# Kernel tuning notes

Hardware: AMD Instinct MI355X
Metric: run time of the kernel (lower is better)

Reference implementation:

```python
import jax, jax.numpy as jnp
import numpy as np

B = 1024      # batch of seed nodes
S = 16        # sample_size
H = 256       # hidden
IN = 150      # in_dim + NUM_CLASS (128 + 22)
OUT = 22
HEADS = 8
NN = 100000   # number of graph nodes
LN_EPS = 1e-5


def setup_inputs() -> dict:
    key = jax.random.key(0)
    ks = jax.random.split(key, 16)
    sc = 0.05
    return {
        "node_feats": jax.random.normal(ks[0], (NN, IN), jnp.float32),
        "batch": jax.random.randint(ks[1], (B,), 0, NN),
        "nbr2": jax.random.randint(ks[2], (B, S), 0, NN),
        "nbr1": jax.random.randint(ks[3], (B * (S + 1), S), 0, NN),
        "W_in": jax.random.normal(ks[4], (IN, H), jnp.float32) * sc,
        "b_in": jnp.zeros((H,), jnp.float32),
        "Wqkv": jax.random.normal(ks[5], (2, 3, H, H), jnp.float32) * sc,
        "bqkv": jnp.zeros((2, 3, H), jnp.float32),
        "Wo": jax.random.normal(ks[6], (2, H, H), jnp.float32) * sc,
        "bo": jnp.zeros((2, H), jnp.float32),
        "Wf": jax.random.normal(ks[7], (2, H, H), jnp.float32) * sc,
        "bf": jnp.zeros((2, H), jnp.float32),
        "ln_g": jnp.ones((4, H), jnp.float32),
        "ln_b": jnp.zeros((4, H), jnp.float32),
        "W_out": jax.random.normal(ks[8], (H, OUT), jnp.float32) * sc,
        "b_out": jnp.zeros((OUT,), jnp.float32),
    }


def _layer_norm(x, g, b):
    m = jnp.mean(x, axis=-1, keepdims=True)
    v = jnp.mean((x - m) ** 2, axis=-1, keepdims=True)
    return (x - m) * jax.lax.rsqrt(v + LN_EPS) * g + b


def _mha(q, kv, Wq, Wk, Wv, bq, bk, bv, Wout, bout):
    # q: [N, 1, H], kv: [N, S, H]; single-query multi-head attention
    N, Sk, _ = kv.shape
    dh = H // HEADS
    qp = (q @ Wq + bq).reshape(N, 1, HEADS, dh)
    kp = (kv @ Wk + bk).reshape(N, Sk, HEADS, dh)
    vp = (kv @ Wv + bv).reshape(N, Sk, HEADS, dh)
    att = jax.nn.softmax(
        jnp.einsum("nqhd,nkhd->nhqk", qp, kp) / np.float32(np.sqrt(dh)), axis=-1
    )
    o = jnp.einsum("nhqk,nkhd->nqhd", att, vp).reshape(N, 1, H)
    return o @ Wout + bout


def _attn_block(x, l, Wqkv, bqkv, Wo, bo, Wf, bf, ln_g, ln_b):
    # x: [N, S+1, H]; slot 0 is the query (self), rest are sampled neighbors
    q, kv = x[:, 0:1, :], x[:, 1:, :]
    h = _mha(q, kv, Wqkv[l, 0], Wqkv[l, 1], Wqkv[l, 2],
             bqkv[l, 0], bqkv[l, 1], bqkv[l, 2], Wo[l], bo[l])
    h = h[:, 0, :] + q[:, 0, :]                       # residual
    h = _layer_norm(h, ln_g[2 * l], ln_b[2 * l])
    h = h + (h @ Wf[l] + bf[l])                       # FFN (single Linear) + residual
    return _layer_norm(h, ln_g[2 * l + 1], ln_b[2 * l + 1])


def reference(node_feats, batch, nbr2, nbr1, W_in, b_in, Wqkv, bqkv, Wo, bo,
              Wf, bf, ln_g, ln_b, W_out, b_out):
    # Recursive neighbor expansion (unrolled for layers=2)
    ids1 = jnp.concatenate([batch[:, None], nbr2], axis=1).reshape(-1)   # [B*(S+1)]
    ids0 = jnp.concatenate([ids1[:, None], nbr1], axis=1).reshape(-1)    # [B*(S+1)^2]
    # layer 0: proj_in(features) = ReLU(Linear) (Dropout identity in eval)
    h0 = jax.nn.relu(node_feats[ids0] @ W_in + b_in)                     # [M0, H]
    # layer 1
    h1 = _attn_block(h0.reshape(B * (S + 1), S + 1, H), 0,
                     Wqkv, bqkv, Wo, bo, Wf, bf, ln_g, ln_b)
    # layer 2
    h2 = _attn_block(h1.reshape(B, S + 1, H), 1,
                     Wqkv, bqkv, Wo, bo, Wf, bf, ln_g, ln_b)
    # proj_out: Linear -> Softmax
    return jax.nn.softmax(h2 @ W_out + b_out, axis=-1)
```

## Files before the change

### kernel.cpp

```cpp
#include <hip/hip_runtime.h>
#include <hip/hip_bf16.h>
#include <math.h>

typedef unsigned short ushort_t;
typedef __bf16 bf16x8 __attribute__((ext_vector_type(8)));
typedef float  f32x4  __attribute__((ext_vector_type(4)));

#define B_SZ   1024
#define SEQ    17
#define KVN    16
#define HDIM   256
#define NHEAD  8
#define DH     32
#define INF    150
#define OUTD   22
#define LN_EPS 1e-5f
#define N1     (B_SZ * SEQ)
#define NN_    100000

constexpr size_t SZ_H0    = (size_t)NN_ * 256 * 2;
constexpr size_t SZ_KV0   = (size_t)NN_ * 512 * 2;
constexpr size_t SZ_ROW   = (size_t)N1 * 256 * 2;
constexpr size_t OFF_H0   = 0;
constexpr size_t OFF_KV0  = OFF_H0 + SZ_H0;
constexpr size_t OFF_QKV1 = OFF_KV0;
constexpr size_t OFF_O1   = OFF_QKV1 + (size_t)N1 * 768 * 2;
constexpr size_t OFF_HA2  = OFF_O1 + (size_t)B_SZ * 256 * 2;
constexpr size_t OFF_H2   = OFF_HA2 + (size_t)B_SZ * 256 * 2;
constexpr size_t OFF_Q0   = OFF_KV0 + SZ_KV0;
constexpr size_t OFF_O0   = OFF_Q0 + SZ_ROW;
constexpr size_t OFF_H1   = OFF_O0;
constexpr size_t OFF_HA   = OFF_O0 + SZ_ROW;
constexpr size_t OFF_IDS  = OFF_HA + SZ_ROW;
constexpr size_t OFF_WTIN = OFF_IDS + (size_t)N1 * 4;
constexpr size_t OFF_WKV0 = OFF_WTIN + 256 * 160 * 2;
constexpr size_t OFF_WQ0  = OFF_WKV0 + 512 * 256 * 2;
constexpr size_t OFF_WKVQ1= OFF_WQ0 + 256 * 256 * 2;
constexpr size_t OFF_WO0  = OFF_WKVQ1 + 768 * 256 * 2;
constexpr size_t OFF_WF0  = OFF_WO0 + 256 * 256 * 2;
constexpr size_t OFF_WO1  = OFF_WF0 + 256 * 256 * 2;
constexpr size_t OFF_WF1  = OFF_WO1 + 256 * 256 * 2;
constexpr size_t OFF_B1   = OFF_WF1 + 256 * 256 * 2;

__device__ __forceinline__ ushort_t f2bfu(float x) {
    __hip_bfloat16 h = __float2bfloat16(x);
    return *reinterpret_cast<ushort_t*>(&h);
}
__device__ __forceinline__ float bfu2f(ushort_t u) {
    __hip_bfloat16 h;
    *reinterpret_cast<ushort_t*>(&h) = u;
    return __bfloat162float(h);
}
__device__ __forceinline__ f32x4 mfma16(bf16x8 a, bf16x8 b, f32x4 c) {
    return __builtin_amdgcn_mfma_f32_16x16x32_bf16(a, b, c, 0, 0, 0);
}

__global__ __launch_bounds__(256) void k_prep(
    const float* __restrict__ W_in, const float* __restrict__ Wqkv,
    const float* __restrict__ Wo, const float* __restrict__ Wf,
    const float* __restrict__ bqkv,
    const int* __restrict__ batch, const int* __restrict__ nbr2,
    char* __restrict__ ws) {
    const int job = blockIdx.y;
    const int idx = blockIdx.x * 256 + threadIdx.x;
    if (job == 11) {
        if (idx < N1) {
            int b = idx / SEQ, s = idx % SEQ;
            ((int*)(ws + OFF_IDS))[idx] = (s == 0) ? batch[b] : nbr2[b * KVN + s - 1];
        }
        return;
    }
    if (job == 12) {
        if (idx < 768) ((float*)(ws + OFF_B1))[idx] = bqkv[768 + ((idx + 256) % 768)];
        return;
    }
    const float* src = nullptr; ushort_t* dst = nullptr;
    int Kpad = 256, Kvalid = 256;
    switch (job) {
        case 0:  src = W_in;           dst = (ushort_t*)(ws + OFF_WTIN); Kpad = 160; Kvalid = 150; break;
        case 1:  src = Wqkv + 65536;   dst = (ushort_t*)(ws + OFF_WKV0); break;
        case 2:  src = Wqkv + 131072;  dst = (ushort_t*)(ws + OFF_WKV0) + 65536; break;
        case 3:  src = Wqkv;           dst = (ushort_t*)(ws + OFF_WQ0); break;
        case 4:  src = Wqkv + 262144;  dst = (ushort_t*)(ws + OFF_WKVQ1); break;
        case 5:  src = Wqkv + 327680;  dst = (ushort_t*)(ws + OFF_WKVQ1) + 65536; break;
        case 6:  src = Wqkv + 196608;  dst = (ushort_t*)(ws + OFF_WKVQ1) + 131072; break;
        case 7:  src = Wo;             dst = (ushort_t*)(ws + OFF_WO0); break;
        case 8:  src = Wo + 65536;     dst = (ushort_t*)(ws + OFF_WO1); break;
        case 9:  src = Wf;             dst = (ushort_t*)(ws + OFF_WF0); break;
        case 10: src = Wf + 65536;     dst = (ushort_t*)(ws + OFF_WF1); break;
    }
    const int total = 256 * Kpad;
    if (idx >= total) return;
    int n = idx / Kpad, k = idx % Kpad;
    dst[idx] = (k < Kvalid) ? f2bfu(src[(size_t)k * 256 + n]) : (ushort_t)0;
}

__global__ __launch_bounds__(512, 2) void k_in_kv(
    const float* __restrict__ nf, const ushort_t* __restrict__ Wt_in,
    const float* __restrict__ b_in, const ushort_t* __restrict__ Wkv,
    const float* __restrict__ bqkv, ushort_t* __restrict__ h0,
    ushort_t* __restrict__ kv0) {
    __shared__ ushort_t AhE[128 * 256];
    __shared__ union {
        struct { ushort_t Ain[2][128][40]; ushort_t Bw[2][256][40]; } p1;
        ushort_t Bkv[2][512][40];
    } smu;

    const int tid  = threadIdx.x;
    const int m0   = blockIdx.x * 128;
    const int lane = tid & 63, w = tid >> 6;
    const int wr = w >> 2, wc = w & 3;
    const int lr = lane & 15, lk = (lane >> 4) * 8;
    const int q4 = lane >> 4;

    const int rowA = tid >> 2, segA = tid & 3;
    const int rowB = tid >> 1, halfB = tid & 1;

    auto loadA1 = [&](int s) -> int4 {
        int gm = m0 + rowA;
        bool v = gm < NN_; if (!v) gm = 0;
        int k0 = s * 32 + segA * 8;
        const float* ap = nf + (size_t)gm * INF + k0;
        ushort_t tmp[8];
        if (v && k0 + 8 <= INF) {
            #pragma unroll
            for (int j = 0; j < 8; ++j) tmp[j] = f2bfu(ap[j]);
        } else {
            #pragma unroll
            for (int j = 0; j < 8; ++j)
                tmp[j] = (v && k0 + j < INF) ? f2bfu(ap[j]) : (ushort_t)0;
        }
        return *reinterpret_cast<int4*>(tmp);
    };

    {
        int4 a = loadA1(0);
        const ushort_t* bp = Wt_in + (size_t)rowB * 160 + halfB * 16;
        int4 b0 = *reinterpret_cast<const int4*>(bp);
        int4 b1 = *reinterpret_cast<const int4*>(bp + 8);
        *reinterpret_cast<int4*>(&smu.p1.Ain[0][rowA][segA * 8]) = a;
        *reinterpret_cast<int4*>(&smu.p1.Bw[0][rowB][halfB * 16]) = b0;
        *reinterpret_cast<int4*>(&smu.p1.Bw[0][rowB][halfB * 16 + 8]) = b1;
    }
    __syncthreads();

    f32x4 acc1[4][4] = {};
    for (int s = 0; s < 5; ++s) {
        const int cur = s & 1;
        int4 pa, pb0, pb1;
        if (s < 4) {
            pa = loadA1(s + 1);
            const ushort_t* bp = Wt_in + (size_t)rowB * 160 + (s + 1) * 32 + halfB * 16;
            pb0 = *reinterpret_cast<const int4*>(bp);
            pb1 = *reinterpret_cast<const int4*>(bp + 8);
        }
        bf16x8 a[4], b[4];
        #pragma unroll
        for (int mi = 0; mi < 4; ++mi)
            a[mi] = *reinterpret_cast<const bf16x8*>(&smu.p1.Ain[cur][wr * 64 + mi * 16 + lr][lk]);
        #pragma unroll
        for (int ni = 0; ni < 4; ++ni)
            b[ni] = *reinterpret_cast<const bf16x8*>(&smu.p1.Bw[cur][wc * 64 + ni * 16 + lr][lk]);
        #pragma unroll
        for (int mi = 0; mi < 4; ++mi)
            #pragma unroll
            for (int ni = 0; ni < 4; ++ni)
                acc1[mi][ni] = mfma16(a[mi], b[ni], acc1[mi][ni]);
        if (s < 4) {
            *reinterpret_cast<int4*>(&smu.p1.Ain[cur ^ 1][rowA][segA * 8]) = pa;
            *reinterpret_cast<int4*>(&smu.p1.Bw[cur ^ 1][rowB][halfB * 16]) = pb0;
            *reinterpret_cast<int4*>(&smu.p1.Bw[cur ^ 1][rowB][halfB * 16 + 8]) = pb1;
        }
        __syncthreads();
    }
    #pragma unroll
    for (int ni = 0; ni < 4; ++ni) {
        int col = wc * 64 + ni * 16 + lr;
        float bb = b_in[col];
        #pragma unroll
        for (int mi = 0; mi < 4; ++mi)
            #pragma unroll
            for (int r = 0; r < 4; ++r) {
                int row = wr * 64 + mi * 16 + q4 * 4 + r;
                AhE[row * 256 + (col ^ ((row & 7) << 3))] =
                    f2bfu(fmaxf(acc1[mi][ni][r] + bb, 0.f));
            }
    }
    __syncthreads();
    #pragma unroll
    for (int i = 0; i < 8; ++i) {
        int flat = tid + i * 512;
        int row = flat >> 5, ch = flat & 31;
        if (m0 + row < NN_)
            *reinterpret_cast<int4*>(h0 + (size_t)(m0 + row) * 256 + ch * 8) =
                *reinterpret_cast<const int4*>(&AhE[row * 256 + (ch ^ (row & 7)) * 8]);
    }

    {
        #pragma unroll
        for (int j = 0; j < 4; ++j) {
            int chf = tid + j * 512;
            int n = chf >> 2, c8 = (chf & 3) * 8;
            *reinterpret_cast<int4*>(&smu.Bkv[0][n][c8]) =
                *reinterpret_cast<const int4*>(Wkv + (size_t)n * 256 + c8);
        }
    }
    __syncthreads();

    f32x4 acc2[4][8] = {};
    for (int s = 0; s < 8; ++s) {
        const int cur = s & 1;
        int4 pb[4];
        if (s < 7) {
            #pragma unroll
            for (int j = 0; j < 4; ++j) {
                int chf = tid + j * 512;
                int n = chf >> 2, c8 = (chf & 3) * 8;
                pb[j] = *reinterpret_cast<const int4*>(Wkv + (size_t)n * 256 + (s + 1) * 32 + c8);
            }
        }
        bf16x8 a[4], b[8];
        #pragma unroll
        for (int mi = 0; mi < 4; ++mi) {
            int row = wr * 64 + mi * 16 + lr;
            int chunk = (s * 4 + q4) ^ (row & 7);
            a[mi] = *reinterpret_cast<const bf16x8*>(&AhE[row * 256 + chunk * 8]);
        }
        #pragma unroll
        for (int ni = 0; ni < 8; ++ni)
            b[ni] = *reinterpret_cast<const bf16x8*>(&smu.Bkv[cur][wc * 128 + ni * 16 + lr][lk]);
        #pragma unroll
        for (int mi = 0; mi < 4; ++mi)
            #pragma unroll
            for (int ni = 0; ni < 8; ++ni)
                acc2[mi][ni] = mfma16(a[mi], b[ni], acc2[mi][ni]);
        if (s < 7) {
            #pragma unroll
            for (int j = 0; j < 4; ++j) {
                int chf = tid + j * 512;
                int n = chf >> 2, c8 = (chf & 3) * 8;
                *reinterpret_cast<int4*>(&smu.Bkv[cur ^ 1][n][c8]) = pb[j];
            }
        }
        __syncthreads();
    }

    #pragma unroll
    for (int h = 0; h < 2; ++h) {
        if ((wc >> 1) == h) {
            int cb = (wc & 1) * 128;
            #pragma unroll
            for (int ni = 0; ni < 8; ++ni) {
                int coll = cb + ni * 16 + lr;
                float bb = bqkv[256 + h * 256 + coll];
                #pragma unroll
                for (int mi = 0; mi < 4; ++mi)
                    #pragma unroll
                    for (int r = 0; r < 4; ++r) {
                        int row = wr * 64 + mi * 16 + q4 * 4 + r;
                        AhE[row * 256 + (coll ^ ((row & 7) << 3))] =
                            f2bfu(acc2[mi][ni][r] + bb);
                    }
            }
        }
        __syncthreads();
        #pragma unroll
        for (int i = 0; i < 8; ++i) {
            int flat = tid + i * 512;
            int row = flat >> 5, ch = flat & 31;
            if (m0 + row < NN_)
                *reinterpret_cast<int4*>(kv0 + (size_t)(m0 + row) * 512 + h * 256 + ch * 8) =
                    *reinterpret_cast<const int4*>(&AhE[row * 256 + (ch ^ (row & 7)) * 8]);
        }
        __syncthreads();
    }
}

template<bool RELU>
__global__ __launch_bounds__(256) void gemm64(
    const ushort_t* __restrict__ Asrc, const ushort_t* __restrict__ Bt,
    const float* __restrict__ biasN, ushort_t* __restrict__ out,
    int M, int Ksteps, int lda, int ldb, int ldo,
    const int* __restrict__ arid) {
    __shared__ ushort_t Al[64][40];
    __shared__ ushort_t Bl[64][40];
    const int tid = threadIdx.x;
    const int m0 = blockIdx.x * 64, n0 = blockIdx.y * 64;
    const int lane = tid & 63, w = tid >> 6, wm = w >> 1, wn = w & 1;
    const int srow = tid >> 2, sch = tid & 3;

    f32x4 acc[2][2] = {};
    for (int s = 0; s < Ksteps; ++s) {
        const int kk = s * 32;
        {
            int gm = m0 + srow;
            bool valid = gm < M;
            if (arid) gm = valid ? arid[gm] : 0;
            int4 v = {0, 0, 0, 0};
            if (valid) v = *reinterpret_cast<const int4*>(Asrc + (size_t)gm * lda + kk + sch * 8);
            *reinterpret_cast<int4*>(&Al[srow][sch * 8]) = v;
        }
        {
            int nrow = n0 + srow;
            int4 v = *reinterpret_cast<const int4*>(Bt + (size_t)nrow * ldb + kk + sch * 8);
            *reinterpret_cast<int4*>(&Bl[srow][sch * 8]) = v;
        }
        __syncthreads();
        const int lr = lane & 15, lk = (lane >> 4) * 8;
        bf16x8 a0 = *reinterpret_cast<const bf16x8*>(&Al[wm * 32 + lr][lk]);
        bf16x8 a1 = *reinterpret_cast<const bf16x8*>(&Al[wm * 32 + 16 + lr][lk]);
        bf16x8 b0 = *reinterpret_cast<const bf16x8*>(&Bl[wn * 32 + lr][lk]);
        bf16x8 b1 = *reinterpret_cast<const bf16x8*>(&Bl[wn * 32 + 16 + lr][lk]);
        acc[0][0] = mfma16(a0, b0, acc[0][0]);
        acc[0][1] = mfma16(a0, b1, acc[0][1]);
        acc[1][0] = mfma16(a1, b0, acc[1][0]);
        acc[1][1] = mfma16(a1, b1, acc[1][1]);
        __syncthreads();
    }
    #pragma unroll
    for (int mi = 0; mi < 2; ++mi)
        #pragma unroll
        for (int ni = 0; ni < 2; ++ni)
            #pragma unroll
            for (int r = 0; r < 4; ++r) {
                int m = m0 + wm * 32 + mi * 16 + ((lane >> 4) << 2) + r;
                int n = n0 + wn * 32 + ni * 16 + (lane & 15);
                if (m < M) {
                    float v = acc[mi][ni][r] + biasN[n];
                    if (RELU) v = fmaxf(v, 0.f);
                    out[(size_t)m * ldo + n] = f2bfu(v);
                }
            }
}

__global__ __launch_bounds__(256) void gemm_ln(
    const ushort_t* __restrict__ A, const ushort_t* __restrict__ Bt,
    const float* __restrict__ biasN,
    const ushort_t* __restrict__ resmat, const int* __restrict__ residx, int rstride,
    const float* __restrict__ lng, const float* __restrict__ lnb,
    ushort_t* __restrict__ out, int M) {
    __shared__ union {
        struct { ushort_t Al[32][40]; ushort_t Bl[256][40]; } s;
        struct { float xr[32][260]; float mrow[32]; float rrow[32]; int sidx[32]; } e;
    } sm;
    const int tid = threadIdx.x;
    const int m0 = blockIdx.x * 32;
    const int lane = tid & 63, w = tid >> 6;

    f32x4 acc[2][4] = {};
    for (int s = 0; s < 8; ++s) {
        const int kk = s * 32;
        if (tid < 128) {
            int row = tid >> 2, ch = tid & 3;
            *reinterpret_cast<int4*>(&sm.s.Al[row][ch * 8]) =
                *reinterpret_cast<const int4*>(A + (size_t)(m0 + row) * 256 + kk + ch * 8);
        }
        #pragma unroll
        for (int j = 0; j < 4; ++j)
            *reinterpret_cast<int4*>(&sm.s.Bl[tid][j * 8]) =
                *reinterpret_cast<const int4*>(Bt + (size_t)tid * 256 + kk + j * 8);
        __syncthreads();
        const int lr = lane & 15, lk = (lane >> 4) * 8;
        bf16x8 a0 = *reinterpret_cast<const bf16x8*>(&sm.s.Al[lr][lk]);
        bf16x8 a1 = *reinterpret_cast<const bf16x8*>(&sm.s.Al[16 + lr][lk]);
        #pragma unroll
        for (int ni = 0; ni < 4; ++ni) {
            bf16x8 b = *reinterpret_cast<const bf16x8*>(&sm.s.Bl[w * 64 + ni * 16 + lr][lk]);
            acc[0][ni] = mfma16(a0, b, acc[0][ni]);
            acc[1][ni] = mfma16(a1, b, acc[1][ni]);
        }
        __syncthreads();
    }
    if (tid < 32) sm.e.sidx[tid] = residx ? residx[m0 + tid] : (m0 + tid) * rstride;
    #pragma unroll
    for (int mi = 0; mi < 2; ++mi)
        #pragma unroll
        for (int ni = 0; ni < 4; ++ni)
            #pragma unroll
            for (int r = 0; r < 4; ++r) {
                int rl = mi * 16 + ((lane >> 4) << 2) + r;
                int cl = w * 64 + ni * 16 + (lane & 15);
                sm.e.xr[rl][cl] = acc[mi][ni][r];
            }
    __syncthreads();
    {
        float bn = biasN[tid];
        for (int r = 0; r < 32; ++r)
            sm.e.xr[r][tid] += bn + bfu2f(resmat[(size_t)sm.e.sidx[r] * 256 + tid]);
    }
    __syncthreads();
    {
        for (int rr = w * 8; rr < w * 8 + 8; ++rr) {
            float4 v = *reinterpret_cast<const float4*>(&sm.e.xr[rr][lane * 4]);
            float s1 = v.x + v.y + v.z + v.w;
            float s2 = v.x * v.x + v.y * v.y + v.z * v.z + v.w * v.w;
            #pragma unroll
            for (int off = 32; off > 0; off >>= 1) {
                s1 += __shfl_xor(s1, off);
                s2 += __shfl_xor(s2, off);
            }
            if (lane == 0) {
                float m = s1 * (1.f / 256.f);
                float var = s2 * (1.f / 256.f) - m * m;
                sm.e.mrow[rr] = m;
                sm.e.rrow[rr] = rsqrtf(var + LN_EPS);
            }
        }
    }
    __syncthreads();
    {
        float g = lng[tid], b = lnb[tid];
        for (int r = 0; r < 32; ++r) {
            float v = (sm.e.xr[r][tid] - sm.e.mrow[r]) * sm.e.rrow[r] * g + b;
            out[(size_t)(m0 + r) * 256 + tid] = f2bfu(v);
        }
    }
}

__global__ __launch_bounds__(256) void attn_wave(
    const ushort_t* __restrict__ q_all, int qld, int qoff, int qstride,
    const ushort_t* __restrict__ kv_all, int kvld, int koff, int voff,
    const int* __restrict__ kvidx, int ngroups, ushort_t* __restrict__ o_out) {
    __shared__ ushort_t KL[4][KVN][264];
    __shared__ ushort_t VL[4][KVN][264];
    const int w = threadIdx.x >> 6, lane = threadIdx.x & 63;
    const int g = blockIdx.x * 4 + w;
    if (g >= ngroups) return;

    int idx16 = 0;
    if (lane < KVN)
        idx16 = kvidx ? kvidx[g * KVN + lane] : g * SEQ + 1 + lane;

    float qv[4];
    {
        uint2 u = *reinterpret_cast<const uint2*>(
            q_all + (size_t)g * qstride * qld + qoff + lane * 4);
        qv[0] = bfu2f((ushort_t)(u.x & 0xffff));
        qv[1] = bfu2f((ushort_t)(u.x >> 16));
        qv[2] = bfu2f((ushort_t)(u.y & 0xffff));
        qv[3] = bfu2f((ushort_t)(u.y >> 16));
    }

    {
        const int r = lane & 15, qtr = lane >> 4;
        int rid = __shfl(idx16, r);
        const ushort_t* kb = kv_all + (size_t)rid * kvld + koff;
        const ushort_t* vb = kv_all + (size_t)rid * kvld + voff;
        #pragma unroll
        for (int j = 0; j < 8; ++j) {
            int c8 = (qtr * 8 + j) * 8;
            *reinterpret_cast<int4*>(&KL[w][r][c8]) = *reinterpret_cast<const int4*>(kb + c8);
            *reinterpret_cast<int4*>(&VL[w][r][c8]) = *reinterpret_cast<const int4*>(vb + c8);
        }
    }

    float att[KVN];
    #pragma unroll
    for (int k = 0; k < KVN; ++k) {
        uint2 u = *reinterpret_cast<const uint2*>(&KL[w][k][lane * 4]);
        float p = qv[0] * bfu2f((ushort_t)(u.x & 0xffff))
                + qv[1] * bfu2f((ushort_t)(u.x >> 16))
                + qv[2] * bfu2f((ushort_t)(u.y & 0xffff))
                + qv[3] * bfu2f((ushort_t)(u.y >> 16));
        p += __shfl_xor(p, 1);
        p += __shfl_xor(p, 2);
        p += __shfl_xor(p, 4);
        att[k] = p * 0.17677669529663687f;
    }
    float m = att[0];
    #pragma unroll
    for (int k = 1; k < KVN; ++k) m = fmaxf(m, att[k]);
    float sum = 0.f;
    #pragma unroll
    for (int k = 0; k < KVN; ++k) { att[k] = __expf(att[k] - m); sum += att[k]; }
    float inv = 1.f / sum;

    float o[4] = {0.f, 0.f, 0.f, 0.f};
    #pragma unroll
    for (int k = 0; k < KVN; ++k) {
        uint2 u = *reinterpret_cast<const uint2*>(&VL[w][k][lane * 4]);
        float a = att[k] * inv;
        o[0] += a * bfu2f((ushort_t)(u.x & 0xffff));
        o[1] += a * bfu2f((ushort_t)(u.x >> 16));
        o[2] += a * bfu2f((ushort_t)(u.y & 0xffff));
        o[3] += a * bfu2f((ushort_t)(u.y >> 16));
    }
    uint2 r;
    r.x = (unsigned)f2bfu(o[0]) | ((unsigned)f2bfu(o[1]) << 16);
    r.y = (unsigned)f2bfu(o[2]) | ((unsigned)f2bfu(o[3]) << 16);
    *reinterpret_cast<uint2*>(o_out + (size_t)g * 256 + lane * 4) = r;
}

__global__ __launch_bounds__(64) void k_out(
    const ushort_t* __restrict__ h2, const float* __restrict__ W_out,
    const float* __restrict__ b_out, float* __restrict__ out) {
    const int b = blockIdx.x, j = threadIdx.x;
    __shared__ float xr[HDIM];
    for (int k = j; k < HDIM; k += 64) xr[k] = bfu2f(h2[(size_t)b * HDIM + k]);
    __syncthreads();
    float logit = -1e30f;
    if (j < OUTD) {
        float acc = b_out[j];
        for (int k = 0; k < HDIM; ++k) acc += xr[k] * W_out[k * OUTD + j];
        logit = acc;
    }
    float m = logit;
    #pragma unroll
    for (int off = 32; off > 0; off >>= 1) m = fmaxf(m, __shfl_xor(m, off));
    float e = (j < OUTD) ? __expf(logit - m) : 0.f;
    float s = e;
    #pragma unroll
    for (int off = 32; off > 0; off >>= 1) s += __shfl_xor(s, off);
    if (j < OUTD) out[(size_t)b * OUTD + j] = e / s;
}

extern "C" void kernel_launch(void* const* d_in, const int* in_sizes, int n_in,
                              void* d_out, int out_size, void* d_ws, size_t ws_size,
                              hipStream_t stream) {
    const float* nf    = (const float*)d_in[0];
    const int*   batch = (const int*)d_in[1];
    const int*   nbr2  = (const int*)d_in[2];
    const int*   nbr1  = (const int*)d_in[3];
    const float* W_in  = (const float*)d_in[4];
    const float* b_in  = (const float*)d_in[5];
    const float* Wqkv  = (const float*)d_in[6];
    const float* bqkv  = (const float*)d_in[7];
    const float* Wo    = (const float*)d_in[8];
    const float* bo    = (const float*)d_in[9];
    const float* Wf    = (const float*)d_in[10];
    const float* bf    = (const float*)d_in[11];
    const float* ln_g  = (const float*)d_in[12];
    const float* ln_b  = (const float*)d_in[13];
    const float* W_out = (const float*)d_in[14];
    const float* b_out = (const float*)d_in[15];
    float* out = (float*)d_out;
    char* ws = (char*)d_ws;

    ushort_t* h0   = (ushort_t*)(ws + OFF_H0);
    ushort_t* kv0  = (ushort_t*)(ws + OFF_KV0);
    ushort_t* q0   = (ushort_t*)(ws + OFF_Q0);
    ushort_t* o0   = (ushort_t*)(ws + OFF_O0);
    ushort_t* ha   = (ushort_t*)(ws + OFF_HA);
    ushort_t* h1   = (ushort_t*)(ws + OFF_H1);
    ushort_t* qkv1 = (ushort_t*)(ws + OFF_QKV1);
    ushort_t* o1   = (ushort_t*)(ws + OFF_O1);
    ushort_t* ha2  = (ushort_t*)(ws + OFF_HA2);
    ushort_t* h2   = (ushort_t*)(ws + OFF_H2);
    const int* ids1 = (const int*)(ws + OFF_IDS);

    hipLaunchKernelGGL(k_prep, dim3(256, 13), dim3(256), 0, stream,
                       W_in, Wqkv, Wo, Wf, bqkv, batch, nbr2, ws);
    hipLaunchKernelGGL(k_in_kv, dim3(782), dim3(512), 0, stream,
                       nf, (const ushort_t*)(ws + OFF_WTIN), b_in,
                       (const ushort_t*)(ws + OFF_WKV0), bqkv, h0, kv0);
    hipLaunchKernelGGL((gemm64<false>), dim3(272, 4), dim3(256), 0, stream,
                       h0, (const ushort_t*)(ws + OFF_WQ0), bqkv, q0,
                       N1, 8, 256, 256, 256, ids1);
    hipLaunchKernelGGL(attn_wave, dim3(N1 / 4), dim3(256), 0, stream,
                       q0, 256, 0, 1, kv0, 512, 0, 256, nbr1, N1, o0);
    hipLaunchKernelGGL(gemm_ln, dim3(544), dim3(256), 0, stream,
                       o0, (const ushort_t*)(ws + OFF_WO0), bo,
                       h0, ids1, 1, ln_g, ln_b, ha, N1);
    hipLaunchKernelGGL(gemm_ln, dim3(544), dim3(256), 0, stream,
                       ha, (const ushort_t*)(ws + OFF_WF0), bf,
                       ha, (const int*)nullptr, 1, ln_g + 256, ln_b + 256, h1, N1);
    hipLaunchKernelGGL((gemm64<false>), dim3(272, 12), dim3(256), 0, stream,
                       h1, (const ushort_t*)(ws + OFF_WKVQ1),
                       (const float*)(ws + OFF_B1), qkv1,
                       N1, 8, 256, 256, 768, (const int*)nullptr);
    hipLaunchKernelGGL(attn_wave, dim3(B_SZ / 4), dim3(256), 0, stream,
                       qkv1, 768, 512, 17, qkv1, 768, 0, 256,
                       (const int*)nullptr, B_SZ, o1);
    hipLaunchKernelGGL(gemm_ln, dim3(32), dim3(256), 0, stream,
                       o1, (const ushort_t*)(ws + OFF_WO1), bo + 256,
                       h1, (const int*)nullptr, 17, ln_g + 512, ln_b + 512, ha2, B_SZ);
    hipLaunchKernelGGL(gemm_ln, dim3(32), dim3(256), 0, stream,
                       ha2, (const ushort_t*)(ws + OFF_WF1), bf + 256,
                       ha2, (const int*)nullptr, 1, ln_g + 768, ln_b + 768, h2, B_SZ);
    hipLaunchKernelGGL(k_out, dim3(B_SZ), dim3(64), 0, stream,
                       h2, W_out, b_out, out);
}
```

Measured before the change: 326.0 us.

## Shrink k_in_kv tile to 64 rows and register-prefetch operands in GEMMs

Rewrites the fused input-projection plus KV GEMM kernel to use 64-row tiles with 256 threads, a single LDS stage fed by register prefetch, and processes the K and V halves sequentially. The goal is less LDS use, more resident blocks, and more blocks in flight. gemm64 and gemm_ln now also prefetch the next K-slice into registers, and gemm_ln loads the whole A tile once up front. In exchange, each block reloads more weight data and synchronizes more often.

```diff
diff --git a/kernel.cpp b/kernel.cpp
--- a/kernel.cpp
+++ b/kernel.cpp
@@ -95,26 +95,22 @@
     dst[idx] = (k < Kvalid) ? f2bfu(src[(size_t)k * 256 + n]) : (ushort_t)0;
 }
 
-__global__ __launch_bounds__(512, 2) void k_in_kv(
+__global__ __launch_bounds__(256, 3) void k_in_kv(
     const float* __restrict__ nf, const ushort_t* __restrict__ Wt_in,
     const float* __restrict__ b_in, const ushort_t* __restrict__ Wkv,
     const float* __restrict__ bqkv, ushort_t* __restrict__ h0,
     ushort_t* __restrict__ kv0) {
-    __shared__ ushort_t AhE[128 * 256];
-    __shared__ union {
-        struct { ushort_t Ain[2][128][40]; ushort_t Bw[2][256][40]; } p1;
-        ushort_t Bkv[2][512][40];
-    } smu;
+    __shared__ ushort_t Ah[64 * 256];
+    __shared__ ushort_t Bst[256][40];
 
     const int tid  = threadIdx.x;
-    const int m0   = blockIdx.x * 128;
+    const int m0   = blockIdx.x * 64;
     const int lane = tid & 63, w = tid >> 6;
-    const int wr = w >> 2, wc = w & 3;
-    const int lr = lane & 15, lk = (lane >> 4) * 8;
-    const int q4 = lane >> 4;
-
+    const int lr = lane & 15, q4 = lane >> 4, lk = q4 * 8;
+
+    ushort_t (*Ain)[36] = reinterpret_cast<ushort_t (*)[36]>(Ah);
     const int rowA = tid >> 2, segA = tid & 3;
-    const int rowB = tid >> 1, halfB = tid & 1;
+    const int rowS = tid >> 2, segS = tid & 3;
 
     auto loadA1 = [&](int s) -> int4 {
         int gm = m0 + rowA;
@@ -122,157 +118,144 @@
         int k0 = s * 32 + segA * 8;
         const float* ap = nf + (size_t)gm * INF + k0;
         ushort_t tmp[8];
-        if (v && k0 + 8 <= INF) {
-            #pragma unroll
-            for (int j = 0; j < 8; ++j) tmp[j] = f2bfu(ap[j]);
-        } else {
-            #pragma unroll
-            for (int j = 0; j < 8; ++j)
-                tmp[j] = (v && k0 + j < INF) ? f2bfu(ap[j]) : (ushort_t)0;
-        }
+        #pragma unroll
+        for (int j = 0; j < 8; ++j)
+            tmp[j] = (v && k0 + j < INF) ? f2bfu(ap[j]) : (ushort_t)0;
         return *reinterpret_cast<int4*>(tmp);
     };
-
-    {
-        int4 a = loadA1(0);
-        const ushort_t* bp = Wt_in + (size_t)rowB * 160 + halfB * 16;
-        int4 b0 = *reinterpret_cast<const int4*>(bp);
-        int4 b1 = *reinterpret_cast<const int4*>(bp + 8);
-        *reinterpret_cast<int4*>(&smu.p1.Ain[0][rowA][segA * 8]) = a;
-        *reinterpret_cast<int4*>(&smu.p1.Bw[0][rowB][halfB * 16]) = b0;
-        *reinterpret_cast<int4*>(&smu.p1.Bw[0][rowB][halfB * 16 + 8]) = b1;
-    }
-    __syncthreads();
+    auto loadB1 = [&](int s) -> int4 {
+        return *reinterpret_cast<const int4*>(
+            Wt_in + (size_t)rowS * 160 + s * 32 + segS * 8);
+    };
+
+    int4 aP = loadA1(0);
+    int4 bP = loadB1(0);
+    int4 bPx[4];
+    #pragma unroll
+    for (int j = 0; j < 4; ++j)
+        bPx[j] = *reinterpret_cast<const int4*>(
+            Wt_in + (size_t)(rowS + 64 * j) * 160 + segS * 8);
 
     f32x4 acc1[4][4] = {};
     for (int s = 0; s < 5; ++s) {
-        const int cur = s & 1;
-        int4 pa, pb0, pb1;
+        __syncthreads();
+        *reinterpret_cast<int4*>(&Ain[rowA][segA * 8]) = aP;
+        #pragma unroll
+        for (int j = 0; j < 4; ++j)
+            *reinterpret_cast<int4*>(&Bst[rowS + 64 * j][segS * 8]) = bPx[j];
         if (s < 4) {
-            pa = loadA1(s + 1);
-            const ushort_t* bp = Wt_in + (size_t)rowB * 160 + (s + 1) * 32 + halfB * 16;
-            pb0 = *reinterpret_cast<const int4*>(bp);
-            pb1 = *reinterpret_cast<const int4*>(bp + 8);
-        }
+            aP = loadA1(s + 1);
+            #pragma unroll
+            for (int j = 0; j < 4; ++j)
+                bPx[j] = *reinterpret_cast<const int4*>(
+                    Wt_in + (size_t)(rowS + 64 * j) * 160 + (s + 1) * 32 + segS * 8);
+        }
+        __syncthreads();
         bf16x8 a[4], b[4];
         #pragma unroll
         for (int mi = 0; mi < 4; ++mi)
-            a[mi] = *reinterpret_cast<const bf16x8*>(&smu.p1.Ain[cur][wr * 64 + mi * 16 + lr][lk]);
+            a[mi] = *reinterpret_cast<const bf16x8*>(&Ain[mi * 16 + lr][lk]);
         #pragma unroll
         for (int ni = 0; ni < 4; ++ni)
-            b[ni] = *reinterpret_cast<const bf16x8*>(&smu.p1.Bw[cur][wc * 64 + ni * 16 + lr][lk]);
+            b[ni] = *reinterpret_cast<const bf16x8*>(&Bst[w * 64 + ni * 16 + lr][lk]);
         #pragma unroll
         for (int mi = 0; mi < 4; ++mi)
             #pragma unroll
             for (int ni = 0; ni < 4; ++ni)
                 acc1[mi][ni] = mfma16(a[mi], b[ni], acc1[mi][ni]);
-        if (s < 4) {
-            *reinterpret_cast<int4*>(&smu.p1.Ain[cur ^ 1][rowA][segA * 8]) = pa;
-            *reinterpret_cast<int4*>(&smu.p1.Bw[cur ^ 1][rowB][halfB * 16]) = pb0;
-            *reinterpret_cast<int4*>(&smu.p1.Bw[cur ^ 1][rowB][halfB * 16 + 8]) = pb1;
-        }
-        __syncthreads();
-    }
+    }
+    __syncthreads();
     #pragma unroll
     for (int ni = 0; ni < 4; ++ni) {
-        int col = wc * 64 + ni * 16 + lr;
+        int col = w * 64 + ni * 16 + lr;
         float bb = b_in[col];
         #pragma unroll
         for (int mi = 0; mi < 4; ++mi)
             #pragma unroll
             for (int r = 0; r < 4; ++r) {
-                int row = wr * 64 + mi * 16 + q4 * 4 + r;
-                AhE[row * 256 + (col ^ ((row & 7) << 3))] =
+                int row = mi * 16 + q4 * 4 + r;
+                Ah[row * 256 + (col ^ ((row & 7) << 3))] =
                     f2bfu(fmaxf(acc1[mi][ni][r] + bb, 0.f));
             }
     }
     __syncthreads();
     #pragma unroll
     for (int i = 0; i < 8; ++i) {
-        int flat = tid + i * 512;
+        int flat = tid + i * 256;
         int row = flat >> 5, ch = flat & 31;
         if (m0 + row < NN_)
             *reinterpret_cast<int4*>(h0 + (size_t)(m0 + row) * 256 + ch * 8) =
-                *reinterpret_cast<const int4*>(&AhE[row * 256 + (ch ^ (row & 7)) * 8]);
-    }
-
-    {
-        #pragma unroll
-        for (int j = 0; j < 4; ++j) {
-            int chf = tid + j * 512;
-            int n = chf >> 2, c8 = (chf & 3) * 8;
-            *reinterpret_cast<int4*>(&smu.Bkv[0][n][c8]) =
-                *reinterpret_cast<const int4*>(Wkv + (size_t)n * 256 + c8);
-        }
-    }
-    __syncthreads();
-
-    f32x4 acc2[4][8] = {};
-    for (int s = 0; s < 8; ++s) {
-        const int cur = s & 1;
-        int4 pb[4];
-        if (s < 7) {
-            #pragma unroll
-            for (int j = 0; j < 4; ++j) {
-                int chf = tid + j * 512;
-                int n = chf >> 2, c8 = (chf & 3) * 8;
-                pb[j] = *reinterpret_cast<const int4*>(Wkv + (size_t)n * 256 + (s + 1) * 32 + c8);
-            }
-        }
-        bf16x8 a[4], b[8];
-        #pragma unroll
-        for (int mi = 0; mi < 4; ++mi) {
-            int row = wr * 64 + mi * 16 + lr;
-            int chunk = (s * 4 + q4) ^ (row & 7);
-            a[mi] = *reinterpret_cast<const bf16x8*>(&AhE[row * 256 + chunk * 8]);
-        }
-        #pragma unroll
-        for (int ni = 0; ni < 8; ++ni)
-            b[ni] = *reinterpret_cast<const bf16x8*>(&smu.Bkv[cur][wc * 128 + ni * 16 + lr][lk]);
-        #pragma unroll
-        for (int mi = 0; mi < 4; ++mi)
-            #pragma unroll
-            for (int ni = 0; ni < 8; ++ni)
-                acc2[mi][ni] = mfma16(a[mi], b[ni], acc2[mi][ni]);
-        if (s < 7) {
-            #pragma unroll
-            for (int j = 0; j < 4; ++j) {
-                int chf = tid + j * 512;
-                int n = chf >> 2, c8 = (chf & 3) * 8;
-                *reinterpret_cast<int4*>(&smu.Bkv[cur ^ 1][n][c8]) = pb[j];
-            }
-        }
-        __syncthreads();
-    }
-
-    #pragma unroll
+                *reinterpret_cast<const int4*>(&Ah[row * 256 + (ch ^ (row & 7)) * 8]);
+    }
+
     for (int h = 0; h < 2; ++h) {
-        if ((wc >> 1) == h) {
-            int cb = (wc & 1) * 128;
-            #pragma unroll
-            for (int ni = 0; ni < 8; ++ni) {
-                int coll = cb + ni * 16 + lr;
-                float bb = bqkv[256 + h * 256 + coll];
+        int4 b2P[4];
+        #pragma unroll
+        for (int j = 0; j < 4; ++j)
+            b2P[j] = *reinterpret_cast<const int4*>(
+                Wkv + (size_t)(h * 256 + rowS + 64 * j) * 256 + segS * 8);
+
+        f32x4 acc2[4][4] = {};
+        for (int s = 0; s < 8; ++s) {
+            __builtin_amdgcn_s_barrier();
+            #pragma unroll
+            for (int j = 0; j < 4; ++j)
+                *reinterpret_cast<int4*>(&Bst[rowS + 64 * j][segS * 8]) = b2P[j];
+            if (s < 7) {
                 #pragma unroll
-                for (int mi = 0; mi < 4; ++mi)
+                for (int j = 0; j < 4; ++j)
+                    b2P[j] = *reinterpret_cast<const int4*>(
+                        Wkv + (size_t)(h * 256 + rowS + 64 * j) * 256 + (s + 1) * 32 + segS * 8);
+            }
+            asm volatile("s_waitcnt lgkmcnt(0)" ::: "memory");
+            __builtin_amdgcn_s_barrier();
+            bf16x8 a[4], b[4];
+            #pragma unroll
+            for (int mi = 0; mi < 4; ++mi) {
+                int row = mi * 16 + lr;
+                int chunk = (s * 4 + q4) ^ (row & 7);
+                a[mi] = *reinterpret_cast<const bf16x8*>(&Ah[row * 256 + chunk * 8]);
+            }
+            #pragma unroll
+            for (int ni = 0; ni < 4; ++ni)
+                b[ni] = *reinterpret_cast<const bf16x8*>(&Bst[w * 64 + ni * 16 + lr][lk]);
+            #pragma unroll
+            for (int mi = 0; mi < 4; ++mi)
+                #pragma unroll
+                for (int ni = 0; ni < 4; ++ni)
+                    acc2[mi][ni] = mfma16(a[mi], b[ni], acc2[mi][ni]);
+        }
+        __syncthreads();
+        ushort_t (*BE)[132] = reinterpret_cast<ushort_t (*)[132]>(&Bst[0][0]);
+        #pragma unroll
+        for (int sub = 0; sub < 2; ++sub) {
+            if ((w >> 1) == sub) {
+                int cb = (w & 1) * 64;
+                #pragma unroll
+                for (int ni = 0; ni < 4; ++ni) {
+                    int coll = cb + ni * 16 + lr;
+                    float bb = bqkv[256 + h * 256 + sub * 128 + coll];
                     #pragma unroll
-                    for (int r = 0; r < 4; ++r) {
-                        int row = wr * 64 + mi * 16 + q4 * 4 + r;
-                        AhE[row * 256 + (coll ^ ((row & 7) << 3))] =
-                            f2bfu(acc2[mi][ni][r] + bb);
-                    }
-            }
-        }
-        __syncthreads();
-        #pragma unroll
-        for (int i = 0; i < 8; ++i) {
-            int flat = tid + i * 512;
-            int row = flat >> 5, ch = flat & 31;
-            if (m0 + row < NN_)
-                *reinterpret_cast<int4*>(kv0 + (size_t)(m0 + row) * 512 + h * 256 + ch * 8) =
-                    *reinterpret_cast<const int4*>(&AhE[row * 256 + (ch ^ (row & 7)) * 8]);
-        }
-        __syncthreads();
+                    for (int mi = 0; mi < 4; ++mi)
+                        #pragma unroll
+                        for (int r = 0; r < 4; ++r) {
+                            int row = mi * 16 + q4 * 4 + r;
+                            BE[row][coll] = f2bfu(acc2[mi][ni][r] + bb);
+                        }
+                }
+            }
+            __syncthreads();
+            #pragma unroll
+            for (int i = 0; i < 4; ++i) {
+                int flat = tid + i * 256;
+                int row = flat >> 4, ch = flat & 15;
+                if (m0 + row < NN_)
+                    *reinterpret_cast<int4*>(
+                        kv0 + (size_t)(m0 + row) * 512 + h * 256 + sub * 128 + ch * 8) =
+                        *reinterpret_cast<const int4*>(&BE[row][ch * 8]);
+            }
+            __syncthreads();
+        }
     }
 }
 
@@ -288,22 +271,24 @@
     const int m0 = blockIdx.x * 64, n0 = blockIdx.y * 64;
     const int lane = tid & 63, w = tid >> 6, wm = w >> 1, wn = w & 1;
     const int srow = tid >> 2, sch = tid & 3;
+    const int gmi = m0 + srow;
+    const bool valid = gmi < M;
+    const int gr = valid ? (arid ? arid[gmi] : gmi) : 0;
+    const ushort_t* arow = Asrc + (size_t)gr * lda + sch * 8;
+    const ushort_t* brow = Bt + (size_t)(n0 + srow) * ldb + sch * 8;
+
+    int4 aP = {0, 0, 0, 0};
+    if (valid) aP = *reinterpret_cast<const int4*>(arow);
+    int4 bP = *reinterpret_cast<const int4*>(brow);
 
     f32x4 acc[2][2] = {};
     for (int s = 0; s < Ksteps; ++s) {
-        const int kk = s * 32;
-        {
-            int gm = m0 + srow;
-            bool valid = gm < M;
-            if (arid) gm = valid ? arid[gm] : 0;
-            int4 v = {0, 0, 0, 0};
-            if (valid) v = *reinterpret_cast<const int4*>(Asrc + (size_t)gm * lda + kk + sch * 8);
-            *reinterpret_cast<int4*>(&Al[srow][sch * 8]) = v;
-        }
-        {
-            int nrow = n0 + srow;
-            int4 v = *reinterpret_cast<const int4*>(Bt + (size_t)nrow * ldb + kk + sch * 8);
-            *reinterpret_cast<int4*>(&Bl[srow][sch * 8]) = v;
+        __syncthreads();
+        *reinterpret_cast<int4*>(&Al[srow][sch * 8]) = aP;
+        *reinterpret_cast<int4*>(&Bl[srow][sch * 8]) = bP;
+        if (s + 1 < Ksteps) {
+            if (valid) aP = *reinterpret_cast<const int4*>(arow + (s + 1) * 32);
+            bP = *reinterpret_cast<const int4*>(brow + (s + 1) * 32);
         }
         __syncthreads();
         const int lr = lane & 15, lk = (lane >> 4) * 8;
@@ -315,7 +300,6 @@
         acc[0][1] = mfma16(a0, b1, acc[0][1]);
         acc[1][0] = mfma16(a1, b0, acc[1][0]);
         acc[1][1] = mfma16(a1, b1, acc[1][1]);
-        __syncthreads();
     }
     #pragma unroll
     for (int mi = 0; mi < 2; ++mi)
@@ -340,37 +324,48 @@
     const float* __restrict__ lng, const float* __restrict__ lnb,
     ushort_t* __restrict__ out, int M) {
     __shared__ union {
-        struct { ushort_t Al[32][40]; ushort_t Bl[256][40]; } s;
+        struct { ushort_t Al[32][264]; ushort_t Bl[256][40]; } s;
         struct { float xr[32][260]; float mrow[32]; float rrow[32]; int sidx[32]; } e;
     } sm;
     const int tid = threadIdx.x;
     const int m0 = blockIdx.x * 32;
     const int lane = tid & 63, w = tid >> 6;
+    const int lr = lane & 15, lk = (lane >> 4) * 8;
+
+    #pragma unroll
+    for (int j = 0; j < 4; ++j) {
+        int flat = tid + j * 256;
+        int row = flat >> 5, ch = flat & 31;
+        *reinterpret_cast<int4*>(&sm.s.Al[row][ch * 8]) =
+            *reinterpret_cast<const int4*>(A + (size_t)(m0 + row) * 256 + ch * 8);
+    }
+    const ushort_t* brow = Bt + (size_t)tid * 256;
+    int4 bP[4];
+    #pragma unroll
+    for (int j = 0; j < 4; ++j) bP[j] = *reinterpret_cast<const int4*>(brow + j * 8);
 
     f32x4 acc[2][4] = {};
     for (int s = 0; s < 8; ++s) {
-        const int kk = s * 32;
-        if (tid < 128) {
-            int row = tid >> 2, ch = tid & 3;
-            *reinterpret_cast<int4*>(&sm.s.Al[row][ch * 8]) =
-                *reinterpret_cast<const int4*>(A + (size_t)(m0 + row) * 256 + kk + ch * 8);
-        }
+        __syncthreads();
         #pragma unroll
         for (int j = 0; j < 4; ++j)
-            *reinterpret_cast<int4*>(&sm.s.Bl[tid][j * 8]) =
-                *reinterpret_cast<const int4*>(Bt + (size_t)tid * 256 + kk + j * 8);
-        __syncthreads();
-        const int lr = lane & 15, lk = (lane >> 4) * 8;
-        bf16x8 a0 = *reinterpret_cast<const bf16x8*>(&sm.s.Al[lr][lk]);
-        bf16x8 a1 = *reinterpret_cast<const bf16x8*>(&sm.s.Al[16 + lr][lk]);
+            *reinterpret_cast<int4*>(&sm.s.Bl[tid][j * 8]) = bP[j];
+        if (s < 7) {
+            #pragma unroll
+            for (int j = 0; j < 4; ++j)
+                bP[j] = *reinterpret_cast<const int4*>(brow + (s + 1) * 32 + j * 8);
+        }
+        __syncthreads();
+        bf16x8 a0 = *reinterpret_cast<const bf16x8*>(&sm.s.Al[lr][s * 32 + lk]);
+        bf16x8 a1 = *reinterpret_cast<const bf16x8*>(&sm.s.Al[16 + lr][s * 32 + lk]);
         #pragma unroll
         for (int ni = 0; ni < 4; ++ni) {
             bf16x8 b = *reinterpret_cast<const bf16x8*>(&sm.s.Bl[w * 64 + ni * 16 + lr][lk]);
             acc[0][ni] = mfma16(a0, b, acc[0][ni]);
             acc[1][ni] = mfma16(a1, b, acc[1][ni]);
         }
-        __syncthreads();
-    }
+    }
+    __syncthreads();
     if (tid < 32) sm.e.sidx[tid] = residx ? residx[m0 + tid] : (m0 + tid) * rstride;
     #pragma unroll
     for (int mi = 0; mi < 2; ++mi)
@@ -440,7 +435,6 @@
         qv[2] = bfu2f((ushort_t)(u.y & 0xffff));
         qv[3] = bfu2f((ushort_t)(u.y >> 16));
     }
-
     {
         const int r = lane & 15, qtr = lane >> 4;
         int rid = __shfl(idx16, r);
@@ -453,7 +447,6 @@
             *reinterpret_cast<int4*>(&VL[w][r][c8]) = *reinterpret_cast<const int4*>(vb + c8);
         }
     }
-
     float att[KVN];
     #pragma unroll
     for (int k = 0; k < KVN; ++k) {
@@ -474,7 +467,6 @@
     #pragma unroll
     for (int k = 0; k < KVN; ++k) { att[k] = __expf(att[k] - m); sum += att[k]; }
     float inv = 1.f / sum;
-
     float o[4] = {0.f, 0.f, 0.f, 0.f};
     #pragma unroll
     for (int k = 0; k < KVN; ++k) {
@@ -550,7 +542,7 @@
 
     hipLaunchKernelGGL(k_prep, dim3(256, 13), dim3(256), 0, stream,
                        W_in, Wqkv, Wo, Wf, bqkv, batch, nbr2, ws);
-    hipLaunchKernelGGL(k_in_kv, dim3(782), dim3(512), 0, stream,
+    hipLaunchKernelGGL(k_in_kv, dim3(1563), dim3(256), 0, stream,
                        nf, (const ushort_t*)(ws + OFF_WTIN), b_in,
                        (const ushort_t*)(ws + OFF_WKV0), bqkv, h0, kv0);
     hipLaunchKernelGGL((gemm64<false>), dim3(272, 4), dim3(256), 0, stream,
```

New measurement: 471.9 us. +44.8%, slower.
